# Optimization experiments

Hardware: AMD Instinct MI355X
Metric: run time of the kernel (lower is better)

Reference implementation:

```python
import jax, jax.numpy as jnp
import numpy as np

N_NODES = 100000
N_EDGES = 1200000
N_GRAPHS = 100  # hardcoded batch_size=100 in the original module


def gcn_conv(x, src, dst, W, b, n):
    """PyG GCNConv: x' = D^{-1/2} (A+I) D^{-1/2} (x W) + b, with self-loops appended."""
    x = x @ W  # [n, out]
    loop = jnp.arange(n, dtype=src.dtype)
    s = jnp.concatenate([src, loop])
    d = jnp.concatenate([dst, loop])
    deg = jax.ops.segment_sum(jnp.ones_like(d, dtype=x.dtype), d, num_segments=n)
    dinv = jax.lax.rsqrt(deg)  # deg >= 1 because of self-loops
    norm = dinv[s] * dinv[d]  # [E+n]
    out = jax.ops.segment_sum(x[s] * norm[:, None], d, num_segments=n)
    return out + b


def setup_inputs() -> dict:
    key = jax.random.key(0)
    ks = jax.random.split(key, 20)
    x = jax.random.normal(ks[0], (N_NODES, 5), dtype=jnp.float32)
    edge_index = jax.random.randint(ks[1], (2, N_EDGES), 0, N_NODES, dtype=jnp.int64)
    batch = jnp.sort(jax.random.randint(ks[2], (N_NODES,), 0, N_GRAPHS, dtype=jnp.int64))

    def lin(k, i, o):
        kw, kb = jax.random.split(k)
        W = jax.random.normal(kw, (i, o), dtype=jnp.float32) * (1.0 / np.sqrt(i))
        b = jax.random.normal(kb, (o,), dtype=jnp.float32) * 0.01
        return W, b

    W1, b1 = lin(ks[3], 5, 32)
    W2, b2 = lin(ks[4], 32, 64)
    nn1_W, nn1_b = lin(ks[5], 64, 124)
    nn2_W, nn2_b = lin(ks[6], 124 * 4, 64)
    W4, b4 = lin(ks[7], 64, 32)
    nn3_W, nn3_b = lin(ks[8], 32, 16)
    nn4_W, nn4_b = lin(ks[9], 16, 1)
    return {
        "x": x, "edge_index": edge_index, "batch": batch,
        "W1": W1, "b1": b1, "W2": W2, "b2": b2,
        "nn1_W": nn1_W, "nn1_b": nn1_b, "nn2_W": nn2_W, "nn2_b": nn2_b,
        "W4": W4, "b4": b4, "nn3_W": nn3_W, "nn3_b": nn3_b,
        "nn4_W": nn4_W, "nn4_b": nn4_b,
    }


def reference(x, edge_index, batch, W1, b1, W2, b2, nn1_W, nn1_b, nn2_W, nn2_b,
              W4, b4, nn3_W, nn3_b, nn4_W, nn4_b):
    src, dst = edge_index[0], edge_index[1]
    h = jax.nn.relu(gcn_conv(x, src, dst, W1, b1, N_NODES))
    h = jax.nn.relu(gcn_conv(h, src, dst, W2, b2, N_NODES))
    h = h @ nn1_W + nn1_b  # [N, 124]

    # four-way scatter pooling over graph ids
    cnt = jax.ops.segment_sum(jnp.ones((N_NODES,), h.dtype), batch, num_segments=N_GRAPHS)
    nonempty = (cnt > 0)[:, None]
    a = jax.ops.segment_max(h, batch, num_segments=N_GRAPHS)
    a = jnp.where(nonempty, a, 0.0)
    b_ = jax.ops.segment_min(h, batch, num_segments=N_GRAPHS)
    b_ = jnp.where(nonempty, b_, 0.0)
    c = jax.ops.segment_sum(h, batch, num_segments=N_GRAPHS)
    d = c / jnp.maximum(cnt, 1.0)[:, None]

    g = jax.nn.relu(jnp.concatenate([a, b_, c, d], axis=1))  # [100, 496]
    g = g @ nn2_W + nn2_b  # [100, 64]

    # conv4 over self-loop-only edge_index on the 100 pooled graph nodes
    loop = jnp.arange(N_GRAPHS)
    g = jax.nn.relu(gcn_conv(g, loop, loop, W4, b4, N_GRAPHS))
    g = jax.nn.relu(g @ nn3_W + nn3_b)
    return g @ nn4_W + nn4_b  # [100, 1]
```

## Files before the change

kernel.cpp:

```cpp
#include <hip/hip_runtime.h>
#include <hip/hip_bf16.h>
#include <math.h>

#define N_NODES  100000
#define N_EDGES  1200000
#define N_GRAPHS 100
#define SCAN_B   1024
#define XRNG     ((N_NODES + 7) / 8)
#define PARTS    16

__global__ void k_degslot(const int* __restrict__ dst, int* __restrict__ deg,
                          int* __restrict__ slotpos, int e) {
    int i = blockIdx.x * blockDim.x + threadIdx.x;
    if (i < e) slotpos[i] = atomicAdd(&deg[dst[i]], 1);
}

__global__ __launch_bounds__(256) void k_fill_x(
    const int* __restrict__ src, const int* __restrict__ dst,
    const int* __restrict__ slotpos, const int* __restrict__ row_ptr,
    int* __restrict__ csr_src, int e, int nchunk) {
    int r = blockIdx.x & 7;
    int chunk = blockIdx.x >> 3;
    int lo = r * XRNG;
    int per = (e + nchunk - 1) / nchunk;
    int beg = chunk * per;
    int end = beg + per < e ? beg + per : e;
    for (int i = beg + threadIdx.x; i < end; i += 256) {
        int d = dst[i];
        if ((unsigned)(d - lo) < (unsigned)XRNG)
            csr_src[row_ptr[d] + slotpos[i]] = src[i];
    }
}

__global__ void k_block_sums(const int* __restrict__ deg, int* __restrict__ bsum, int n) {
    int i = blockIdx.x * SCAN_B + threadIdx.x;
    int v = (i < n) ? deg[i] : 0;
    #pragma unroll
    for (int d = 32; d > 0; d >>= 1) v += __shfl_xor(v, d);
    __shared__ int wsum[SCAN_B / 64];
    int lane = threadIdx.x & 63, w = threadIdx.x >> 6;
    if (lane == 0) wsum[w] = v;
    __syncthreads();
    if (threadIdx.x == 0) {
        int s = 0;
        #pragma unroll
        for (int k = 0; k < SCAN_B / 64; k++) s += wsum[k];
        bsum[blockIdx.x] = s;
    }
}

__global__ void k_scan_bsums(int* __restrict__ bsum, int nb) {
    __shared__ int s[256];
    int t = threadIdx.x;
    int v = (t < nb) ? bsum[t] : 0;
    s[t] = v;
    __syncthreads();
    for (int d = 1; d < 256; d <<= 1) {
        int u = (t >= d) ? s[t - d] : 0;
        __syncthreads();
        s[t] += u;
        __syncthreads();
    }
    if (t < nb) bsum[t] = s[t] - v;
}

__global__ void k_scan_final(const int* __restrict__ deg, const int* __restrict__ bsum,
                             int* __restrict__ row_ptr, float* __restrict__ dinv,
                             int n, int n_edges) {
    int b = blockIdx.x;
    int i = b * SCAN_B + threadIdx.x;
    int v = (i < n) ? deg[i] : 0;
    int lane = threadIdx.x & 63, w = threadIdx.x >> 6;
    int inc = v;
    #pragma unroll
    for (int d = 1; d < 64; d <<= 1) {
        int u = __shfl_up(inc, d);
        if (lane >= d) inc += u;
    }
    __shared__ int wsum[SCAN_B / 64];
    __shared__ int woff[SCAN_B / 64];
    if (lane == 63) wsum[w] = inc;
    __syncthreads();
    if (threadIdx.x == 0) {
        int s = 0;
        #pragma unroll
        for (int k = 0; k < SCAN_B / 64; k++) { woff[k] = s; s += wsum[k]; }
    }
    __syncthreads();
    int excl = bsum[b] + woff[w] + (inc - v);
    if (i < n) {
        row_ptr[i] = excl;
        dinv[i] = rsqrtf((float)(v + 1));
    }
    if (b == 0 && threadIdx.x == 0) row_ptr[n] = n_edges;
}

__global__ void k_y0(const float* __restrict__ x, const float* __restrict__ dinv,
                     float* __restrict__ y0, int n) {
    int idx = blockIdx.x * blockDim.x + threadIdx.x;
    int node = idx >> 3, f = idx & 7;
    if (node >= n) return;
    float v = (f < 5) ? x[node * 5 + f] * dinv[node] : 0.f;
    y0[node * 8 + f] = v;
}

__global__ __launch_bounds__(256) void k_agg1(
    const int* __restrict__ row_ptr, const int* __restrict__ csr_src,
    const float* __restrict__ y0, const float* __restrict__ dinv,
    const float* __restrict__ W1, const float* __restrict__ b1,
    float* __restrict__ y1, int n) {
    int wave = (blockIdx.x * blockDim.x + threadIdx.x) >> 6;
    if (wave >= n) return;
    int lane = threadIdx.x & 63;
    int f = lane & 7, ec = lane >> 3;
    int start = row_ptr[wave], end = row_ptr[wave + 1];
    float acc = 0.f;
    for (int e = start + ec; e < end; e += 8) {
        int s = csr_src[e];
        acc += y0[s * 8 + f];
    }
    if (ec == 0) acc += y0[wave * 8 + f];
    acc += __shfl_down(acc, 32);
    acc += __shfl_down(acc, 16);
    acc += __shfl_down(acc, 8);
    float di = dinv[wave];
    float s0[5];
    #pragma unroll
    for (int k = 0; k < 5; k++) s0[k] = __shfl(acc, k) * di;
    int fo = lane & 31;
    float hv = b1[fo];
    #pragma unroll
    for (int k = 0; k < 5; k++) hv += s0[k] * W1[k * 32 + fo];
    hv = hv > 0.f ? hv : 0.f;
    if (lane < 32) y1[wave * 32 + lane] = hv * di;
}

__global__ __launch_bounds__(256) void k_agg2g(
    const int* __restrict__ row_ptr, const int* __restrict__ csr_src,
    const float* __restrict__ y1, const float* __restrict__ dinv,
    float* __restrict__ sv, int n) {
    int wave = (blockIdx.x * blockDim.x + threadIdx.x) >> 6;
    if (wave >= n) return;
    int lane = threadIdx.x & 63;
    int f = lane & 31, hh = lane >> 5;
    int start = row_ptr[wave], end = row_ptr[wave + 1];
    float a0 = 0.f, a1 = 0.f, a2 = 0.f, a3 = 0.f;
    int e = start + hh;
    for (; e + 6 < end; e += 8) {
        int s0 = csr_src[e],     s1i = csr_src[e + 2];
        int s2 = csr_src[e + 4], s3i = csr_src[e + 6];
        a0 += y1[s0 * 32 + f];
        a1 += y1[s1i * 32 + f];
        a2 += y1[s2 * 32 + f];
        a3 += y1[s3i * 32 + f];
    }
    for (; e < end; e += 2) a0 += y1[csr_src[e] * 32 + f];
    float acc = (a0 + a1) + (a2 + a3);
    acc += __shfl_xor(acc, 32);
    acc += y1[wave * 32 + f];
    if (lane < 32) sv[wave * 32 + lane] = acc * dinv[wave];
}

#define LTS 68
__global__ __launch_bounds__(256) void k_l2mm(
    const float* __restrict__ sv, const float* __restrict__ W2,
    const float* __restrict__ b2, const float* __restrict__ nn1W,
    const float* __restrict__ nn1b, float* __restrict__ h, int n) {
    __shared__ float lsW2[32 * 64];
    __shared__ float lsN[64 * 128];
    __shared__ float lsT[64 * LTS];

    int tid = threadIdx.x;
    int nb = blockIdx.x * 64;

    #pragma unroll
    for (int i = 0; i < 8; i++) lsW2[tid + i * 256] = W2[tid + i * 256];
    for (int idx = tid; idx < 64 * 124; idx += 256)
        lsN[(idx / 124) * 128 + (idx % 124)] = nn1W[idx];
    if (tid < 256) lsN[(tid >> 2) * 128 + 124 + (tid & 3)] = 0.f;
    {
        int node = tid >> 2, kq = (tid & 3) * 8;
        float4 v0, v1;
        if (nb + node < n) {
            v0 = *(const float4*)&sv[(size_t)(nb + node) * 32 + kq];
            v1 = *(const float4*)&sv[(size_t)(nb + node) * 32 + kq + 4];
        } else {
            v0 = make_float4(0.f, 0.f, 0.f, 0.f); v1 = v0;
        }
        lsT[(kq + 0) * LTS + node] = v0.x;
        lsT[(kq + 1) * LTS + node] = v0.y;
        lsT[(kq + 2) * LTS + node] = v0.z;
        lsT[(kq + 3) * LTS + node] = v0.w;
        lsT[(kq + 4) * LTS + node] = v1.x;
        lsT[(kq + 5) * LTS + node] = v1.y;
        lsT[(kq + 6) * LTS + node] = v1.z;
        lsT[(kq + 7) * LTS + node] = v1.w;
    }
    __syncthreads();

    int tf = tid & 15;
    int tn = tid >> 4;

    float c1[4][4] = {};
    #pragma unroll 4
    for (int k = 0; k < 32; k++) {
        float4 a = *(const float4*)&lsT[k * LTS + tn * 4];
        float4 w = *(const float4*)&lsW2[k * 64 + tf * 4];
        const float av[4] = {a.x, a.y, a.z, a.w};
        const float wv[4] = {w.x, w.y, w.z, w.w};
        #pragma unroll
        for (int i = 0; i < 4; i++)
            #pragma unroll
            for (int j = 0; j < 4; j++) c1[i][j] += av[i] * wv[j];
    }
    __syncthreads();
    {
        float4 bb = *(const float4*)&b2[tf * 4];
        const float bv[4] = {bb.x, bb.y, bb.z, bb.w};
        #pragma unroll
        for (int j = 0; j < 4; j++) {
            float4 col;
            col.x = fmaxf(c1[0][j] + bv[j], 0.f);
            col.y = fmaxf(c1[1][j] + bv[j], 0.f);
            col.z = fmaxf(c1[2][j] + bv[j], 0.f);
            col.w = fmaxf(c1[3][j] + bv[j], 0.f);
            *(float4*)&lsT[(tf * 4 + j) * LTS + tn * 4] = col;
        }
    }
    __syncthreads();

    float c2a[4][4] = {}, c2b[4][4] = {};
    #pragma unroll 2
    for (int k = 0; k < 64; k++) {
        float4 a  = *(const float4*)&lsT[k * LTS + tn * 4];
        float4 w1 = *(const float4*)&lsN[k * 128 + tf * 4];
        float4 w2 = *(const float4*)&lsN[k * 128 + 64 + tf * 4];
        const float av[4] = {a.x, a.y, a.z, a.w};
        const float w1v[4] = {w1.x, w1.y, w1.z, w1.w};
        const float w2v[4] = {w2.x, w2.y, w2.z, w2.w};
        #pragma unroll
        for (int i = 0; i < 4; i++)
            #pragma unroll
            for (int j = 0; j < 4; j++) {
                c2a[i][j] += av[i] * w1v[j];
                c2b[i][j] += av[i] * w2v[j];
            }
    }
    {
        float4 ba = *(const float4*)&nn1b[tf * 4];
        const float bav[4] = {ba.x, ba.y, ba.z, ba.w};
        float bbv[4] = {0.f, 0.f, 0.f, 0.f};
        if (tf < 15) {
            float4 bb = *(const float4*)&nn1b[64 + tf * 4];
            bbv[0] = bb.x; bbv[1] = bb.y; bbv[2] = bb.z; bbv[3] = bb.w;
        }
        #pragma unroll
        for (int i = 0; i < 4; i++) {
            int node = nb + tn * 4 + i;
            if (node >= n) break;
            float4 oa, ob;
            oa.x = c2a[i][0] + bav[0]; oa.y = c2a[i][1] + bav[1];
            oa.z = c2a[i][2] + bav[2]; oa.w = c2a[i][3] + bav[3];
            *(float4*)&h[(size_t)node * 124 + tf * 4] = oa;
            if (tf < 15) {
                ob.x = c2b[i][0] + bbv[0]; ob.y = c2b[i][1] + bbv[1];
                ob.z = c2b[i][2] + bbv[2]; ob.w = c2b[i][3] + bbv[3];
                *(float4*)&h[(size_t)node * 124 + 64 + tf * 4] = ob;
            }
        }
    }
}

__global__ __launch_bounds__(512) void k_pool_a(
    const float* __restrict__ h, const int* __restrict__ batch,
    float* __restrict__ pmax, float* __restrict__ pmin, float* __restrict__ psum,
    int n) {
    int g = blockIdx.x / PARTS, r = blockIdx.x % PARTS;
    __shared__ int sb[2];
    if (threadIdx.x < 2) {
        int target = g + threadIdx.x;
        int lo = 0, hi = n;
        while (lo < hi) {
            int mid = (lo + hi) >> 1;
            if (batch[mid] < target) lo = mid + 1; else hi = mid;
        }
        sb[threadIdx.x] = lo;
    }
    __syncthreads();
    int start = sb[0], end = sb[1];
    int t = threadIdx.x;
    int f = t & 127, r2 = t >> 7;
    float vmax = -INFINITY, vmin = INFINITY, vsum = 0.f;
    if (f < 124) {
        for (int node = start + r * 4 + r2; node < end; node += PARTS * 4) {
            float v = h[(size_t)node * 124 + f];
            vmax = fmaxf(vmax, v);
            vmin = fminf(vmin, v);
            vsum += v;
        }
    }
    __shared__ float smax[4][128], smin[4][128], ssum[4][128];
    smax[r2][f] = vmax; smin[r2][f] = vmin; ssum[r2][f] = vsum;
    __syncthreads();
    if (r2 == 0) {
        #pragma unroll
        for (int k = 1; k < 4; k++) {
            vmax = fmaxf(vmax, smax[k][f]);
            vmin = fminf(vmin, smin[k][f]);
            vsum += ssum[k][f];
        }
        int idx = (g * PARTS + r) * 128 + f;
        pmax[idx] = vmax; pmin[idx] = vmin; psum[idx] = vsum;
    }
}

__global__ __launch_bounds__(256) void k_head(
    const float* __restrict__ pmax, const float* __restrict__ pmin,
    const float* __restrict__ psum, const int* __restrict__ batch,
    const float* __restrict__ nn2W, const float* __restrict__ nn2b,
    const float* __restrict__ W4,   const float* __restrict__ b4,
    const float* __restrict__ nn3W, const float* __restrict__ nn3b,
    const float* __restrict__ nn4W, const float* __restrict__ nn4b,
    float* __restrict__ out, int n) {
    int g = blockIdx.x, tid = threadIdx.x;
    int lane = tid & 63, w = tid >> 6;
    __shared__ float lg[496];
    __shared__ float part[4][64];
    __shared__ int sb[2];
    if (tid < 2) {
        int target = g + tid;
        int lo = 0, hi = n;
        while (lo < hi) {
            int mid = (lo + hi) >> 1;
            if (batch[mid] < target) lo = mid + 1; else hi = mid;
        }
        sb[tid] = lo;
    }
    __syncthreads();
    if (tid < 124) {
        float vmax = -INFINITY, vmin = INFINITY, vsum = 0.f;
        #pragma unroll 4
        for (int r = 0; r < PARTS; r++) {
            int idx = (g * PARTS + r) * 128 + tid;
            vmax = fmaxf(vmax, pmax[idx]);
            vmin = fminf(vmin, pmin[idx]);
            vsum += psum[idx];
        }
        int cnt = sb[1] - sb[0];
        float a = (cnt > 0) ? vmax : 0.f;
        float b = (cnt > 0) ? vmin : 0.f;
        lg[tid]       = fmaxf(a, 0.f);
        lg[124 + tid] = fmaxf(b, 0.f);
        lg[248 + tid] = fmaxf(vsum, 0.f);
        lg[372 + tid] = fmaxf(vsum / fmaxf((float)cnt, 1.f), 0.f);
    }
    __syncthreads();
    float acc = 0.f;
    int k0 = w * 124;
    #pragma unroll 4
    for (int k = k0; k < k0 + 124; k++)
        acc += lg[k] * nn2W[k * 64 + lane];
    part[w][lane] = acc;
    __syncthreads();
    if (w == 0) {
        float g1 = part[0][lane] + part[1][lane] + part[2][lane] + part[3][lane]
                 + nn2b[lane];
        float acc2 = (lane < 32) ? b4[lane] : 0.f;
        #pragma unroll 8
        for (int k = 0; k < 64; k++) {
            float v = __shfl(g1, k);
            if (lane < 32) acc2 += v * W4[k * 32 + lane];
        }
        float g2 = fmaxf(acc2, 0.f);
        float acc3 = (lane < 16) ? nn3b[lane] : 0.f;
        #pragma unroll 8
        for (int k = 0; k < 32; k++) {
            float v = __shfl(g2, k);
            if (lane < 16) acc3 += v * nn3W[k * 16 + lane];
        }
        float g3 = fmaxf(acc3, 0.f);
        float p = (lane < 16) ? g3 * nn4W[lane] : 0.f;
        p += __shfl_xor(p, 8);
        p += __shfl_xor(p, 4);
        p += __shfl_xor(p, 2);
        p += __shfl_xor(p, 1);
        if (lane == 0) out[g] = p + nn4b[0];
    }
}

extern "C" void kernel_launch(void* const* d_in, const int* in_sizes, int n_in,
                              void* d_out, int out_size, void* d_ws, size_t ws_size,
                              hipStream_t stream) {
    const int N = N_NODES, E = N_EDGES, G = N_GRAPHS;

    const float* x     = (const float*)d_in[0];
    const int*   ei    = (const int*)d_in[1];
    const int*   batch = (const int*)d_in[2];
    const float* W1    = (const float*)d_in[3];
    const float* b1    = (const float*)d_in[4];
    const float* W2    = (const float*)d_in[5];
    const float* b2    = (const float*)d_in[6];
    const float* nn1W  = (const float*)d_in[7];
    const float* nn1b  = (const float*)d_in[8];
    const float* nn2W  = (const float*)d_in[9];
    const float* nn2b  = (const float*)d_in[10];
    const float* W4    = (const float*)d_in[11];
    const float* b4    = (const float*)d_in[12];
    const float* nn3W  = (const float*)d_in[13];
    const float* nn3b  = (const float*)d_in[14];
    const float* nn4W  = (const float*)d_in[15];
    const float* nn4b  = (const float*)d_in[16];

    const int* src = ei;
    const int* dst = ei + E;

    char* ws = (char*)d_ws;
    size_t off = 0;
    auto alloc = [&](size_t bytes) -> char* {
        char* p = ws + off;
        off += (bytes + 255) & ~(size_t)255;
        return p;
    };
    int*   deg     = (int*)  alloc((size_t)N * 4);
    float* dinv    = (float*)alloc((size_t)N * 4);
    int*   row_ptr = (int*)  alloc((size_t)(N + 1) * 4);
    int*   slotpos = (int*)  alloc((size_t)E * 4);
    int*   bsum    = (int*)  alloc(1024 * 4);
    int*   csr_src = (int*)  alloc((size_t)E * 4);
    float* y0      = (float*)alloc((size_t)N * 8 * 4);
    float* y1      = (float*)alloc((size_t)N * 32 * 4);
    float* sv      = (float*)alloc((size_t)N * 32 * 4);
    float* h       = (float*)alloc((size_t)N * 124 * 4);
    float* pmax    = (float*)alloc((size_t)G * PARTS * 128 * 4);
    float* pmin    = (float*)alloc((size_t)G * PARTS * 128 * 4);
    float* psum    = (float*)alloc((size_t)G * PARTS * 128 * 4);
    (void)ws_size;

    float* out = (float*)d_out;

    const int NB = (N + SCAN_B - 1) / SCAN_B;
    const int NCHUNK = 256;

    hipMemsetAsync(deg, 0, (size_t)N * 4, stream);
    k_degslot<<<(E + 255) / 256, 256, 0, stream>>>(dst, deg, slotpos, E);
    k_block_sums<<<NB, SCAN_B, 0, stream>>>(deg, bsum, N);
    k_scan_bsums<<<1, 256, 0, stream>>>(bsum, NB);
    k_scan_final<<<NB, SCAN_B, 0, stream>>>(deg, bsum, row_ptr, dinv, N, E);
    k_fill_x<<<NCHUNK * 8, 256, 0, stream>>>(src, dst, slotpos, row_ptr, csr_src, E, NCHUNK);
    k_y0<<<(N * 8 + 255) / 256, 256, 0, stream>>>(x, dinv, y0, N);
    k_agg1<<<(N + 3) / 4, 256, 0, stream>>>(row_ptr, csr_src, y0, dinv, W1, b1, y1, N);
    k_agg2g<<<(N + 3) / 4, 256, 0, stream>>>(row_ptr, csr_src, y1, dinv, sv, N);
    k_l2mm<<<(N + 63) / 64, 256, 0, stream>>>(sv, W2, b2, nn1W, nn1b, h, N);
    k_pool_a<<<G * PARTS, 512, 0, stream>>>(h, batch, pmax, pmin, psum, N);
    k_head<<<G, 256, 0, stream>>>(pmax, pmin, psum, batch, nn2W, nn2b, W4, b4,
                                  nn3W, nn3b, nn4W, nn4b, out, N);
}
```

Before: 354.3 us.

## Build CSR with shared-memory per-chunk histograms instead of global atomics

Replaces the global atomicAdd degree/slot computation with per-chunk, per-range histograms kept in LDS (12.5K ints per block). Column sums give the degrees, a per-node prefix across chunks gives each chunk's write base, and a second pass re-ranks edges with LDS atomics to scatter the sources into the CSR. This removes contended global atomics, the slotpos array and a memset, at the cost of two extra small kernels, a 32×N count buffer aliased onto h, and dst being read twice by 8 range-filtered passes. Occupancy may be limited by the 50KB of shared memory per block, and only 256 blocks are launched.

```diff
diff --git a/kernel.cpp b/kernel.cpp
--- a/kernel.cpp
+++ b/kernel.cpp
@@ -7,28 +7,69 @@
 #define N_GRAPHS 100
 #define SCAN_B   1024
 #define XRNG     ((N_NODES + 7) / 8)
+#define NCH      32
 #define PARTS    16
 
-__global__ void k_degslot(const int* __restrict__ dst, int* __restrict__ deg,
-                          int* __restrict__ slotpos, int e) {
-    int i = blockIdx.x * blockDim.x + threadIdx.x;
-    if (i < e) slotpos[i] = atomicAdd(&deg[dst[i]], 1);
-}
-
-__global__ __launch_bounds__(256) void k_fill_x(
-    const int* __restrict__ src, const int* __restrict__ dst,
-    const int* __restrict__ slotpos, const int* __restrict__ row_ptr,
-    int* __restrict__ csr_src, int e, int nchunk) {
+__global__ __launch_bounds__(256) void k_hist(
+    const int* __restrict__ dst, int* __restrict__ cnt, int e) {
+    __shared__ int hist[XRNG];
     int r = blockIdx.x & 7;
-    int chunk = blockIdx.x >> 3;
+    int c = blockIdx.x >> 3;
     int lo = r * XRNG;
-    int per = (e + nchunk - 1) / nchunk;
-    int beg = chunk * per;
+    for (int j = threadIdx.x; j < XRNG; j += 256) hist[j] = 0;
+    __syncthreads();
+    int per = (e + NCH - 1) / NCH;
+    int beg = c * per;
     int end = beg + per < e ? beg + per : e;
     for (int i = beg + threadIdx.x; i < end; i += 256) {
         int d = dst[i];
-        if ((unsigned)(d - lo) < (unsigned)XRNG)
-            csr_src[row_ptr[d] + slotpos[i]] = src[i];
+        if ((unsigned)(d - lo) < (unsigned)XRNG) atomicAdd(&hist[d - lo], 1);
+    }
+    __syncthreads();
+    int* base = cnt + (size_t)c * N_NODES + lo;
+    for (int j = threadIdx.x; j < XRNG; j += 256) base[j] = hist[j];
+}
+
+__global__ void k_colsum(const int* __restrict__ cnt, int* __restrict__ deg, int n) {
+    int i = blockIdx.x * blockDim.x + threadIdx.x;
+    if (i >= n) return;
+    int s = 0;
+    #pragma unroll 8
+    for (int c = 0; c < NCH; c++) s += cnt[(size_t)c * n + i];
+    deg[i] = s;
+}
+
+__global__ void k_cbase(int* __restrict__ cnt, const int* __restrict__ row_ptr, int n) {
+    int i = blockIdx.x * blockDim.x + threadIdx.x;
+    if (i >= n) return;
+    int running = row_ptr[i];
+    #pragma unroll 8
+    for (int c = 0; c < NCH; c++) {
+        int t = cnt[(size_t)c * n + i];
+        cnt[(size_t)c * n + i] = running;
+        running += t;
+    }
+}
+
+__global__ __launch_bounds__(256) void k_fill2(
+    const int* __restrict__ src, const int* __restrict__ dst,
+    const int* __restrict__ cbase, int* __restrict__ csr_src, int e) {
+    __shared__ int hist[XRNG];
+    int r = blockIdx.x & 7;
+    int c = blockIdx.x >> 3;
+    int lo = r * XRNG;
+    for (int j = threadIdx.x; j < XRNG; j += 256) hist[j] = 0;
+    __syncthreads();
+    int per = (e + NCH - 1) / NCH;
+    int beg = c * per;
+    int end = beg + per < e ? beg + per : e;
+    const int* cb = cbase + (size_t)c * N_NODES;
+    for (int i = beg + threadIdx.x; i < end; i += 256) {
+        int d = dst[i];
+        if ((unsigned)(d - lo) < (unsigned)XRNG) {
+            int rank = atomicAdd(&hist[d - lo], 1);
+            csr_src[cb[d] + rank] = src[i];
+        }
     }
 }
 
@@ -424,7 +465,6 @@
     int*   deg     = (int*)  alloc((size_t)N * 4);
     float* dinv    = (float*)alloc((size_t)N * 4);
     int*   row_ptr = (int*)  alloc((size_t)(N + 1) * 4);
-    int*   slotpos = (int*)  alloc((size_t)E * 4);
     int*   bsum    = (int*)  alloc(1024 * 4);
     int*   csr_src = (int*)  alloc((size_t)E * 4);
     float* y0      = (float*)alloc((size_t)N * 8 * 4);
@@ -436,17 +476,19 @@
     float* psum    = (float*)alloc((size_t)G * PARTS * 128 * 4);
     (void)ws_size;
 
+    int* cnt = (int*)h;
+
     float* out = (float*)d_out;
 
     const int NB = (N + SCAN_B - 1) / SCAN_B;
-    const int NCHUNK = 256;
-
-    hipMemsetAsync(deg, 0, (size_t)N * 4, stream);
-    k_degslot<<<(E + 255) / 256, 256, 0, stream>>>(dst, deg, slotpos, E);
+
+    k_hist<<<NCH * 8, 256, 0, stream>>>(dst, cnt, E);
+    k_colsum<<<(N + 255) / 256, 256, 0, stream>>>(cnt, deg, N);
     k_block_sums<<<NB, SCAN_B, 0, stream>>>(deg, bsum, N);
     k_scan_bsums<<<1, 256, 0, stream>>>(bsum, NB);
     k_scan_final<<<NB, SCAN_B, 0, stream>>>(deg, bsum, row_ptr, dinv, N, E);
-    k_fill_x<<<NCHUNK * 8, 256, 0, stream>>>(src, dst, slotpos, row_ptr, csr_src, E, NCHUNK);
+    k_cbase<<<(N + 255) / 256, 256, 0, stream>>>(cnt, row_ptr, N);
+    k_fill2<<<NCH * 8, 256, 0, stream>>>(src, dst, cnt, csr_src, E);
     k_y0<<<(N * 8 + 255) / 256, 256, 0, stream>>>(x, dinv, y0, N);
     k_agg1<<<(N + 3) / 4, 256, 0, stream>>>(row_ptr, csr_src, y0, dinv, W1, b1, y1, N);
     k_agg2g<<<(N + 3) / 4, 256, 0, stream>>>(row_ptr, csr_src, y1, dinv, sv, N);
```

Measured after the change: 425.5 us. 1.2x slower.
